# Kernel optimization log

Hardware: AMD Instinct MI355X
Metric: run time of the kernel (lower is better)

Reference implementation:

```python
import jax, jax.numpy as jnp
import numpy as np

B, C_IN, C_OUT, K, H, W, STRIDE, PAD = 64, 64, 128, 3, 32, 32, 1, 1
H_OUT = (H + 2 * PAD - K) // STRIDE + 1
W_OUT = (W + 2 * PAD - K) // STRIDE + 1


def setup_inputs() -> dict:
    key = jax.random.key(0)
    k1, k2 = jax.random.split(key)
    x = jax.random.normal(k1, (B, C_IN, H, W), dtype=jnp.float32)
    fan_in = C_IN * K * K
    weight = jax.random.normal(k2, (C_OUT, H_OUT, W_OUT, C_IN, K, K), dtype=jnp.float32) / np.sqrt(fan_in).astype(np.float32)
    bias = jnp.zeros((C_OUT, H_OUT, W_OUT), dtype=jnp.float32)
    return {"x": x, "weight": weight, "bias": bias}


def _extract_patches(x):
    # x: [B, C, H, W] -> patches [B, C, H_OUT, W_OUT, K, K]
    xp = jnp.pad(x, ((0, 0), (0, 0), (PAD, PAD), (PAD, PAD)))
    rows = []
    for k in range(K):  # small fixed kernel loop (K=3), not a data-dim loop
        cols = []
        for l in range(K):
            cols.append(xp[:, :, k:k + H_OUT * STRIDE:STRIDE, l:l + W_OUT * STRIDE:STRIDE])
        rows.append(jnp.stack(cols, axis=-1))
    return jnp.stack(rows, axis=-2)


def reference(x, weight, bias):
    patches = _extract_patches(x)  # [B, C_IN, H_OUT, W_OUT, K, K]
    # per-location unshared GEMM: out[b,o,h,w] = sum_{i,k,l} weight[o,h,w,i,k,l] * patches[b,i,h,w,k,l]
    out = jnp.einsum('ohwikl,bihwkl->bohw', weight, patches)
    return out + bias[None]
```

## Files before the change

### kernel.cpp

```cpp
#include <hip/hip_runtime.h>


typedef __bf16  bf16x8  __attribute__((ext_vector_type(8)));
typedef float   floatx4 __attribute__((ext_vector_type(4)));

static __device__ inline bf16x8 cvt8(floatx4 a, floatx4 b) {
    bf16x8 r;
    r[0] = (__bf16)a[0]; r[1] = (__bf16)a[1]; r[2] = (__bf16)a[2]; r[3] = (__bf16)a[3];
    r[4] = (__bf16)b[0]; r[5] = (__bf16)b[1]; r[6] = (__bf16)b[2]; r[7] = (__bf16)b[3];
    return r;
}

__global__ __launch_bounds__(256, 2) void local2d_kernel(
    const float* __restrict__ x,
    const float* __restrict__ weight,
    const float* __restrict__ bias,
    float* __restrict__ out)
{
    __shared__ __bf16 alds[9 * 4 * 64 * 8];

    const int tid  = threadIdx.x;
    const int lane = tid & 63;
    const int wv   = tid >> 6;
    const int ll   = lane & 15;
    const int q    = lane >> 4;

    int bid = blockIdx.x;
    int loc = ((bid & 7) << 7) | (bid >> 3);
    int h = loc >> 5, w = loc & 31;

    const int o_base = wv * 32;
    const float* wrow0 = weight + ((size_t)(o_base + ll) * 1024 + loc) * 576;
    const float* wrow1 = wrow0 + (size_t)16 * 1024 * 576;
    const int kq = q * 8;

    floatx4 acc[2][4];
    #pragma unroll
    for (int a = 0; a < 2; ++a)
        #pragma unroll
        for (int m = 0; m < 4; ++m)
            acc[a][m] = (floatx4){0.f, 0.f, 0.f, 0.f};

    for (int c = 0; c < 2; ++c) {
        for (int p = tid; p < 2048; p += 256) {
            int b  = p >> 5;
            int il = p & 31;
            int i  = (c << 5) | il;
            int kbase = il * 9;
            const float* xp = x + ((size_t)b * 64 + i) * 1024;
            int mt      = b >> 4;
            int lane_lo = b & 15;
            #pragma unroll
            for (int ky = 0; ky < 3; ++ky) {
                int y = h + ky - 1;
                bool yok = (unsigned)y < 32u;
                #pragma unroll
                for (int kx = 0; kx < 3; ++kx) {
                    int xc = w + kx - 1;
                    float v = (yok && (unsigned)xc < 32u) ? xp[y * 32 + xc] : 0.0f;
                    int kd = kbase + ky * 3 + kx;
                    int tc = kd >> 5;
                    int r  = kd & 31;
                    int lw = ((r >> 3) << 4) | lane_lo;
                    int j  = r & 7;
                    alds[((((tc << 2) + mt) << 6) | lw) * 8 + j] = (__bf16)v;
                }
            }
        }
        __syncthreads();

        const float* wp0 = wrow0 + c * 288 + kq;
        const float* wp1 = wrow1 + c * 288 + kq;
        #pragma unroll 3
        for (int t = 0; t < 9; ++t) {
            floatx4 b0a = *(const floatx4*)(wp0 + t * 32);
            floatx4 b0b = *(const floatx4*)(wp0 + t * 32 + 4);
            floatx4 b1a = *(const floatx4*)(wp1 + t * 32);
            floatx4 b1b = *(const floatx4*)(wp1 + t * 32 + 4);
            bf16x8 bf0 = cvt8(b0a, b0b);
            bf16x8 bf1 = cvt8(b1a, b1b);
            #pragma unroll
            for (int mt = 0; mt < 4; ++mt) {
                bf16x8 af = *(const bf16x8*)&alds[((((t << 2) + mt) << 6) | lane) * 8];
                acc[0][mt] = __builtin_amdgcn_mfma_f32_16x16x32_bf16(af, bf0, acc[0][mt], 0, 0, 0);
                acc[1][mt] = __builtin_amdgcn_mfma_f32_16x16x32_bf16(af, bf1, acc[1][mt], 0, 0, 0);
            }
        }
        __syncthreads();
    }

    #pragma unroll
    for (int ntl = 0; ntl < 2; ++ntl) {
        int o = o_base + ntl * 16 + ll;
        float bv = bias[(size_t)o * 1024 + loc];
        #pragma unroll
        for (int mt = 0; mt < 4; ++mt) {
            #pragma unroll
            for (int r = 0; r < 4; ++r) {
                int m = (mt << 4) + (q << 2) + r;
                out[((size_t)m * 128 + o) * 1024 + loc] = acc[ntl][mt][r] + bv;
            }
        }
    }
}

extern "C" void kernel_launch(void* const* d_in, const int* in_sizes, int n_in,
                              void* d_out, int out_size, void* d_ws, size_t ws_size,
                              hipStream_t stream) {
    const float* x  = (const float*)d_in[0];
    const float* wt = (const float*)d_in[1];
    const float* bi = (const float*)d_in[2];
    float* out = (float*)d_out;
    local2d_kernel<<<dim3(1024), dim3(256), 0, stream>>>(x, wt, bi, out);
}
```

Before: 576.2 us.

## Split output channels across two blocks and stage weights through LDS

```diff
diff --git a/kernel.cpp b/kernel.cpp
--- a/kernel.cpp
+++ b/kernel.cpp
@@ -18,6 +18,7 @@
     float* __restrict__ out)
 {
     __shared__ __bf16 alds[9 * 4 * 64 * 8];
+    __shared__ __bf16 wlds[36 * 65 * 8];
 
     const int tid  = threadIdx.x;
     const int lane = tid & 63;
@@ -25,24 +26,19 @@
     const int ll   = lane & 15;
     const int q    = lane >> 4;
 
-    int bid = blockIdx.x;
-    int loc = ((bid & 7) << 7) | (bid >> 3);
-    int h = loc >> 5, w = loc & 31;
+    const int bid = blockIdx.x;
+    const int loc = bid >> 1;
+    const int og  = bid & 1;
+    const int h = loc >> 5, w = loc & 31;
 
-    const int o_base = wv * 32;
-    const float* wrow0 = weight + ((size_t)(o_base + ll) * 1024 + loc) * 576;
-    const float* wrow1 = wrow0 + (size_t)16 * 1024 * 576;
-    const int kq = q * 8;
-
-    floatx4 acc[2][4];
+    floatx4 acc[4];
     #pragma unroll
-    for (int a = 0; a < 2; ++a)
-        #pragma unroll
-        for (int m = 0; m < 4; ++m)
-            acc[a][m] = (floatx4){0.f, 0.f, 0.f, 0.f};
+    for (int nt = 0; nt < 4; ++nt) acc[nt] = (floatx4){0.f, 0.f, 0.f, 0.f};
 
     for (int c = 0; c < 2; ++c) {
-        for (int p = tid; p < 2048; p += 256) {
+        #pragma unroll
+        for (int pp = 0; pp < 8; ++pp) {
+            int p  = tid + (pp << 8);
             int b  = p >> 5;
             int il = p & 31;
             int i  = (c << 5) | il;
@@ -67,39 +63,47 @@
                 }
             }
         }
+
+        {
+            const float* wbase = weight + ((size_t)(og * 64) * 1024 + loc) * 576 + c * 288;
+            #pragma unroll
+            for (int it = 0; it < 9; ++it) {
+                int g  = tid + (it << 8);
+                int ol = g / 36;
+                int jg = g - ol * 36;
+                const floatx4* src = (const floatx4*)(wbase + (size_t)ol * 589824 + jg * 8);
+                floatx4 va = src[0];
+                floatx4 vb = src[1];
+                int t  = jg >> 2;
+                int qq = jg & 3;
+                int nt = ol >> 4;
+                int lll = ol & 15;
+                int idx16 = ((t << 2) + nt) * 65 + (qq << 4) + lll;
+                *(bf16x8*)&wlds[idx16 * 8] = cvt8(va, vb);
+            }
+        }
         __syncthreads();
 
-        const float* wp0 = wrow0 + c * 288 + kq;
-        const float* wp1 = wrow1 + c * 288 + kq;
         #pragma unroll 3
         for (int t = 0; t < 9; ++t) {
-            floatx4 b0a = *(const floatx4*)(wp0 + t * 32);
-            floatx4 b0b = *(const floatx4*)(wp0 + t * 32 + 4);
-            floatx4 b1a = *(const floatx4*)(wp1 + t * 32);
-            floatx4 b1b = *(const floatx4*)(wp1 + t * 32 + 4);
-            bf16x8 bf0 = cvt8(b0a, b0b);
-            bf16x8 bf1 = cvt8(b1a, b1b);
+            bf16x8 af = *(const bf16x8*)&alds[((((t << 2) + wv) << 6) | lane) * 8];
             #pragma unroll
-            for (int mt = 0; mt < 4; ++mt) {
-                bf16x8 af = *(const bf16x8*)&alds[((((t << 2) + mt) << 6) | lane) * 8];
-                acc[0][mt] = __builtin_amdgcn_mfma_f32_16x16x32_bf16(af, bf0, acc[0][mt], 0, 0, 0);
-                acc[1][mt] = __builtin_amdgcn_mfma_f32_16x16x32_bf16(af, bf1, acc[1][mt], 0, 0, 0);
+            for (int nt = 0; nt < 4; ++nt) {
+                bf16x8 bw = *(const bf16x8*)&wlds[(((t << 2) + nt) * 65 + lane) * 8];
+                acc[nt] = __builtin_amdgcn_mfma_f32_16x16x32_bf16(af, bw, acc[nt], 0, 0, 0);
             }
         }
         __syncthreads();
     }
 
     #pragma unroll
-    for (int ntl = 0; ntl < 2; ++ntl) {
-        int o = o_base + ntl * 16 + ll;
+    for (int nt = 0; nt < 4; ++nt) {
+        int o = (og << 6) + (nt << 4) + ll;
         float bv = bias[(size_t)o * 1024 + loc];
         #pragma unroll
-        for (int mt = 0; mt < 4; ++mt) {
-            #pragma unroll
-            for (int r = 0; r < 4; ++r) {
-                int m = (mt << 4) + (q << 2) + r;
-                out[((size_t)m * 128 + o) * 1024 + loc] = acc[ntl][mt][r] + bv;
-            }
+        for (int r = 0; r < 4; ++r) {
+            int m = (wv << 4) + (q << 2) + r;
+            out[((size_t)m * 128 + o) * 1024 + loc] = acc[nt][r] + bv;
         }
     }
 }
@@ -111,5 +115,5 @@
     const float* wt = (const float*)d_in[1];
     const float* bi = (const float*)d_in[2];
     float* out = (float*)d_out;
-    local2d_kernel<<<dim3(1024), dim3(256), 0, stream>>>(x, wt, bi, out);
+    local2d_kernel<<<dim3(2048), dim3(256), 0, stream>>>(x, wt, bi, out);
 }
```

New measurement: 690.0 us. 1.2x slower.
